# Optimization experiments

Measured on AMD Instinct MI355X. Metric: run time of the kernel, lower is better.

Reference implementation:

```python
import jax, jax.numpy as jnp
import numpy as np

D_MODEL = 2048
NUM_EXPERTS = 64
TOP_K = 2


def setup_inputs() -> dict:
    key = jax.random.key(0)
    k1, k2 = jax.random.split(key)
    x = jax.random.normal(k1, (4, 4096, D_MODEL), dtype=jnp.float32)
    # nn.Linear(d_model, num_experts) weight: [num_experts, d_model]
    W_gate = jax.random.normal(k2, (NUM_EXPERTS, D_MODEL), dtype=jnp.float32) * (1.0 / np.sqrt(D_MODEL))
    return {"x": x, "W_gate": W_gate}


def reference(x, W_gate):
    # logits: [b, s, e]
    logits = jnp.einsum("bsd,ed->bse", x, W_gate)
    probs = jax.nn.softmax(logits, axis=-1)
    expert_weights, expert_indices = jax.lax.top_k(probs, TOP_K)  # [b, s, k]
    expert_weights = expert_weights / jnp.sum(expert_weights, axis=-1, keepdims=True)
    return expert_indices, expert_weights
```

## Files before the change

kernel.cpp:

```cpp
#include <hip/hip_runtime.h>
#include <math.h>

#define NTOK 16384
#define DK   2048
#define NEXP 64

typedef float f32x4 __attribute__((ext_vector_type(4)));
typedef int   i32x4 __attribute__((ext_vector_type(4)));
typedef short s16x8 __attribute__((ext_vector_type(8)));

__device__ __forceinline__ unsigned short f2bf(float f) {
    union { float f; unsigned u; } v; v.f = f;
    unsigned r = (v.u + 0x7FFFu + ((v.u >> 16) & 1u)) >> 16;
    return (unsigned short)r;
}
__device__ __forceinline__ float bf2f(unsigned short h) {
    union { unsigned u; float f; } v; v.u = ((unsigned)h) << 16;
    return v.f;
}

__global__ __launch_bounds__(256) void wsplit_pack(const float* __restrict__ Wg,
                                                   unsigned short* __restrict__ ws) {
    const int t  = blockIdx.x * 256 + threadIdx.x;
    const int e  = t >> 8;
    const int k  = (t & 255) * 8;
    const int w  = k >> 9;
    const int c  = (k >> 5) & 15;
    const int g  = (k >> 3) & 3;
    const int rr = e & 15;
    const int n  = e >> 4;
    const int lane = g * 16 + rr;

    const float* src = Wg + (size_t)e * DK + k;
    unsigned short p0[8], p1[8], p2[8];
    #pragma unroll
    for (int j = 0; j < 8; ++j) {
        const float f = src[j];
        p0[j] = f2bf(f);  const float r1 = f - bf2f(p0[j]);
        p1[j] = f2bf(r1); const float r2 = r1 - bf2f(p1[j]);
        p2[j] = f2bf(r2);
    }
    const size_t base = ((((size_t)w * 16 + c) * 4 + n) * 3) * 512 + (size_t)lane * 8;
    *(s16x8*)(ws + base)        = *(s16x8*)p0;
    *(s16x8*)(ws + base + 512)  = *(s16x8*)p1;
    *(s16x8*)(ws + base + 1024) = *(s16x8*)p2;
}

__device__ __forceinline__ void gload_lds16(const float* src, float* dst) {
    __builtin_amdgcn_global_load_lds(
        (const __attribute__((address_space(1))) void*)src,
        (__attribute__((address_space(3))) void*)dst, 16, 0, 0);
}

__device__ __forceinline__ unsigned cvtpk(float lo, float hi) {
    unsigned r;
    asm("v_cvt_pk_bf16_f32 %0, %1, %2" : "=v"(r) : "v"(lo), "v"(hi));
    return r;
}

#define SPLIT2(F0, F1, O0, O1, O2) { \
    const unsigned q0 = cvtpk((F0), (F1)); \
    const float s0 = (F0) - __builtin_bit_cast(float, q0 << 16); \
    const float s1 = (F1) - __builtin_bit_cast(float, q0 & 0xFFFF0000u); \
    const unsigned q1 = cvtpk(s0, s1); \
    const float t0 = s0 - __builtin_bit_cast(float, q1 << 16); \
    const float t1 = s1 - __builtin_bit_cast(float, q1 & 0xFFFF0000u); \
    O0 = (int)q0; O1 = (int)q1; O2 = (int)cvtpk(t0, t1); }

#define STAGE_X(c, BUF) { \
    _Pragma("unroll") for (int it = 0; it < 4; ++it) \
        gload_lds16(xsrc + (size_t)it * 8 * DK + (size_t)(c) * 32, \
                    &xs[w][BUF][it * 256]); }

#define ISSUE_B(BS, c) { \
    _Pragma("unroll") for (int n = 0; n < 4; ++n) \
        _Pragma("unroll") for (int p = 0; p < 3; ++p) \
            BS[n][p] = *(const i32x4*)(wbase + ((size_t)(c) * 12 + n * 3 + p) * 512); }

#define CONV_LDS(BUF) { \
    _Pragma("unroll") for (int m = 0; m < 2; ++m) { \
        const int row = rr + 16 * m; \
        const int sw  = row & 7; \
        const float4 xa0 = *(const float4*)&xs[w][BUF][row * 32 + (((g * 2 + 0) ^ sw) << 2)]; \
        const float4 xa1 = *(const float4*)&xs[w][BUF][row * 32 + (((g * 2 + 1) ^ sw) << 2)]; \
        SPLIT2(xa0.x, xa0.y, A[m][0].x, A[m][1].x, A[m][2].x); \
        SPLIT2(xa0.z, xa0.w, A[m][0].y, A[m][1].y, A[m][2].y); \
        SPLIT2(xa1.x, xa1.y, A[m][0].z, A[m][1].z, A[m][2].z); \
        SPLIT2(xa1.z, xa1.w, A[m][0].w, A[m][1].w, A[m][2].w); } }

#define MFMA_TERM(pa, pb, BS) { \
    _Pragma("unroll") for (int m = 0; m < 2; ++m) \
        _Pragma("unroll") for (int n = 0; n < 4; ++n) \
            acc[m][n] = __builtin_amdgcn_mfma_f32_16x16x32_bf16( \
                __builtin_bit_cast(s16x8, A[m][pa]), \
                __builtin_bit_cast(s16x8, BS[n][pb]), acc[m][n], 0, 0, 0); }

#define MFMA_ALL(BS) \
    MFMA_TERM(0, 0, BS) MFMA_TERM(0, 1, BS) MFMA_TERM(1, 0, BS) \
    MFMA_TERM(1, 1, BS) MFMA_TERM(0, 2, BS) MFMA_TERM(2, 0, BS)

#define PHASE(BS, c, NCNT, DO_ISSUE) { \
    asm volatile("s_waitcnt vmcnt(" #NCNT ")" ::: "memory"); \
    __builtin_amdgcn_sched_barrier(0); \
    CONV_LDS((c) & 1); \
    MFMA_ALL(BS); \
    if (DO_ISSUE) { STAGE_X((c) + 2, (c) & 1); ISSUE_B(BS, (c) + 2); } \
    __builtin_amdgcn_sched_barrier(0); }

__global__ __launch_bounds__(256, 2) void topk_router_kernel(
    const float* __restrict__ x,
    const unsigned short* __restrict__ ws,
    float* __restrict__ out)
{
    __shared__ float smem[8704];
    float (*xs)[2][1024] = (float (*)[2][1024])smem;
    float (*lg)[32][68]  = (float (*)[32][68])smem;

    const int tid  = threadIdx.x;
    const int w    = tid >> 6;
    const int lane = tid & 63;
    const int rr   = lane & 15;
    const int g    = lane >> 4;
    const int tok0 = blockIdx.x * 32;

    const int lt = lane >> 3;
    const int lq = lane & 7;
    const float* xsrc = x + (size_t)(tok0 + lt) * DK + w * 512 + ((lq ^ lt) * 4);
    const unsigned short* wbase = ws + (size_t)w * 98304 + (size_t)lane * 8;

    f32x4 acc[2][4];
    #pragma unroll
    for (int m = 0; m < 2; ++m)
        #pragma unroll
        for (int n = 0; n < 4; ++n) acc[m][n] = (f32x4){0.f, 0.f, 0.f, 0.f};

    i32x4 B0[4][3], B1[4][3];
    i32x4 A[2][3];

    STAGE_X(0, 0); ISSUE_B(B0, 0);
    STAGE_X(1, 1); ISSUE_B(B1, 1);

    #pragma unroll 1
    for (int c = 0; c < 14; c += 2) {
        PHASE(B0, c,     16, 1);
        PHASE(B1, c + 1, 16, 1);
    }
    PHASE(B0, 14, 16, 0);
    PHASE(B1, 15,  0, 0);

    __syncthreads();
    #pragma unroll
    for (int m = 0; m < 2; ++m)
        #pragma unroll
        for (int n = 0; n < 4; ++n)
            #pragma unroll
            for (int r = 0; r < 4; ++r)
                lg[w][m * 16 + g * 4 + r][n * 16 + rr] = acc[m][n][r];
    __syncthreads();

    #pragma unroll 1
    for (int t = 0; t < 8; ++t) {
        const int tok = w * 8 + t;
        const float v = lg[0][tok][lane] + lg[1][tok][lane]
                      + lg[2][tok][lane] + lg[3][tok][lane];

        float m1 = v; int i1 = lane;
        #pragma unroll
        for (int off = 32; off > 0; off >>= 1) {
            float ov = __shfl_xor(m1, off);
            int   oi = __shfl_xor(i1, off);
            if (ov > m1 || (ov == m1 && oi < i1)) { m1 = ov; i1 = oi; }
        }
        float m2 = (lane == i1) ? -INFINITY : v; int i2 = lane;
        #pragma unroll
        for (int off = 32; off > 0; off >>= 1) {
            float ov = __shfl_xor(m2, off);
            int   oi = __shfl_xor(i2, off);
            if (ov > m2 || (ov == m2 && oi < i2)) { m2 = ov; i2 = oi; }
        }

        if (lane == 0) {
            const int gtok = tok0 + tok;
            const float e  = expf(m2 - m1);
            const float w1 = 1.0f / (1.0f + e);
            const float w2 = e / (1.0f + e);
            out[gtok * 2 + 0] = (float)i1;
            out[gtok * 2 + 1] = (float)i2;
            out[NTOK * 2 + gtok * 2 + 0] = w1;
            out[NTOK * 2 + gtok * 2 + 1] = w2;
        }
    }
}

extern "C" void kernel_launch(void* const* d_in, const int* in_sizes, int n_in,
                              void* d_out, int out_size, void* d_ws, size_t ws_size,
                              hipStream_t stream) {
    const float* x  = (const float*)d_in[0];
    const float* Wg = (const float*)d_in[1];
    float* out = (float*)d_out;
    unsigned short* ws = (unsigned short*)d_ws;
    hipLaunchKernelGGL(wsplit_pack, dim3(64), dim3(256), 0, stream, Wg, ws);
    hipLaunchKernelGGL(topk_router_kernel, dim3(NTOK / 32), dim3(256), 0, stream,
                       x, ws, out);
}
```

Measured before the change: 47.75 us.

## Split K across eight waves per block and load B just-in-time per phase

Doubles the block to 512 threads so eight waves each handle a 256-wide K slice, with eight phases per wave instead of sixteen. The weight layout is flattened so each wave indexes its K rows directly. B fragments now go into a single register buffer loaded at the start of each phase rather than double-buffered two phases ahead, which cuts register pressure to allow more resident waves. The cross-wave reduction grows to eight partials through a padded LDS buffer. The trade-off is that B load latency is no longer hidden by prefetch.

```diff
diff --git a/kernel.cpp b/kernel.cpp
--- a/kernel.cpp
+++ b/kernel.cpp
@@ -24,8 +24,7 @@
     const int t  = blockIdx.x * 256 + threadIdx.x;
     const int e  = t >> 8;
     const int k  = (t & 255) * 8;
-    const int w  = k >> 9;
-    const int c  = (k >> 5) & 15;
+    const int R  = k >> 5;
     const int g  = (k >> 3) & 3;
     const int rr = e & 15;
     const int n  = e >> 4;
@@ -40,7 +39,7 @@
         p1[j] = f2bf(r1); const float r2 = r1 - bf2f(p1[j]);
         p2[j] = f2bf(r2);
     }
-    const size_t base = ((((size_t)w * 16 + c) * 4 + n) * 3) * 512 + (size_t)lane * 8;
+    const size_t base = (((size_t)R * 4 + n) * 3) * 512 + (size_t)lane * 8;
     *(s16x8*)(ws + base)        = *(s16x8*)p0;
     *(s16x8*)(ws + base + 512)  = *(s16x8*)p1;
     *(s16x8*)(ws + base + 1024) = *(s16x8*)p2;
@@ -72,10 +71,10 @@
         gload_lds16(xsrc + (size_t)it * 8 * DK + (size_t)(c) * 32, \
                     &xs[w][BUF][it * 256]); }
 
-#define ISSUE_B(BS, c) { \
+#define ISSUE_B(BS, R) { \
     _Pragma("unroll") for (int n = 0; n < 4; ++n) \
         _Pragma("unroll") for (int p = 0; p < 3; ++p) \
-            BS[n][p] = *(const i32x4*)(wbase + ((size_t)(c) * 12 + n * 3 + p) * 512); }
+            BS[n][p] = *(const i32x4*)(wbase + ((size_t)(R) * 12 + n * 3 + p) * 512); }
 
 #define CONV_LDS(BUF) { \
     _Pragma("unroll") for (int m = 0; m < 2; ++m) { \
@@ -99,22 +98,22 @@
     MFMA_TERM(0, 0, BS) MFMA_TERM(0, 1, BS) MFMA_TERM(1, 0, BS) \
     MFMA_TERM(1, 1, BS) MFMA_TERM(0, 2, BS) MFMA_TERM(2, 0, BS)
 
-#define PHASE(BS, c, NCNT, DO_ISSUE) { \
+#define PHASE(c, NCNT, DO_X) { \
+    ISSUE_B(BS, R0 + (c)); \
     asm volatile("s_waitcnt vmcnt(" #NCNT ")" ::: "memory"); \
     __builtin_amdgcn_sched_barrier(0); \
     CONV_LDS((c) & 1); \
     MFMA_ALL(BS); \
-    if (DO_ISSUE) { STAGE_X((c) + 2, (c) & 1); ISSUE_B(BS, (c) + 2); } \
+    if (DO_X) STAGE_X((c) + 2, (c) & 1); \
     __builtin_amdgcn_sched_barrier(0); }
 
-__global__ __launch_bounds__(256, 2) void topk_router_kernel(
+__global__ __launch_bounds__(512, 4) void topk_router_kernel(
     const float* __restrict__ x,
     const unsigned short* __restrict__ ws,
     float* __restrict__ out)
 {
-    __shared__ float smem[8704];
+    __shared__ float smem[16640];
     float (*xs)[2][1024] = (float (*)[2][1024])smem;
-    float (*lg)[32][68]  = (float (*)[32][68])smem;
 
     const int tid  = threadIdx.x;
     const int w    = tid >> 6;
@@ -122,11 +121,12 @@
     const int rr   = lane & 15;
     const int g    = lane >> 4;
     const int tok0 = blockIdx.x * 32;
+    const int R0   = w * 8;
 
     const int lt = lane >> 3;
     const int lq = lane & 7;
-    const float* xsrc = x + (size_t)(tok0 + lt) * DK + w * 512 + ((lq ^ lt) * 4);
-    const unsigned short* wbase = ws + (size_t)w * 98304 + (size_t)lane * 8;
+    const float* xsrc = x + (size_t)(tok0 + lt) * DK + w * 256 + ((lq ^ lt) * 4);
+    const unsigned short* wbase = ws + (size_t)lane * 8;
 
     f32x4 acc[2][4];
     #pragma unroll
@@ -134,35 +134,41 @@
         #pragma unroll
         for (int n = 0; n < 4; ++n) acc[m][n] = (f32x4){0.f, 0.f, 0.f, 0.f};
 
-    i32x4 B0[4][3], B1[4][3];
+    i32x4 BS[4][3];
     i32x4 A[2][3];
 
-    STAGE_X(0, 0); ISSUE_B(B0, 0);
-    STAGE_X(1, 1); ISSUE_B(B1, 1);
+    STAGE_X(0, 0);
+    STAGE_X(1, 1);
+
+    PHASE(0, 16, 1);
+    PHASE(1, 16, 1);
+    PHASE(2, 16, 1);
+    PHASE(3, 16, 1);
+    PHASE(4, 16, 1);
+    PHASE(5, 16, 1);
+    PHASE(6, 16, 0);
+    PHASE(7, 12, 0);
+
+    __syncthreads();
+    {
+        float* lg = smem;
+        #pragma unroll
+        for (int m = 0; m < 2; ++m)
+            #pragma unroll
+            for (int n = 0; n < 4; ++n)
+                #pragma unroll
+                for (int r = 0; r < 4; ++r)
+                    lg[(w * 32 + m * 16 + g * 4 + r) * 65 + n * 16 + rr]
+                        = acc[m][n][r];
+    }
+    __syncthreads();
 
     #pragma unroll 1
-    for (int c = 0; c < 14; c += 2) {
-        PHASE(B0, c,     16, 1);
-        PHASE(B1, c + 1, 16, 1);
-    }
-    PHASE(B0, 14, 16, 0);
-    PHASE(B1, 15,  0, 0);
-
-    __syncthreads();
-    #pragma unroll
-    for (int m = 0; m < 2; ++m)
-        #pragma unroll
-        for (int n = 0; n < 4; ++n)
-            #pragma unroll
-            for (int r = 0; r < 4; ++r)
-                lg[w][m * 16 + g * 4 + r][n * 16 + rr] = acc[m][n][r];
-    __syncthreads();
-
-    #pragma unroll 1
-    for (int t = 0; t < 8; ++t) {
-        const int tok = w * 8 + t;
-        const float v = lg[0][tok][lane] + lg[1][tok][lane]
-                      + lg[2][tok][lane] + lg[3][tok][lane];
+    for (int t = 0; t < 4; ++t) {
+        const int tok = w * 4 + t;
+        float v = 0.f;
+        #pragma unroll
+        for (int p = 0; p < 8; ++p) v += smem[(p * 32 + tok) * 65 + lane];
 
         float m1 = v; int i1 = lane;
         #pragma unroll
@@ -200,6 +206,6 @@
     float* out = (float*)d_out;
     unsigned short* ws = (unsigned short*)d_ws;
     hipLaunchKernelGGL(wsplit_pack, dim3(64), dim3(256), 0, stream, Wg, ws);
-    hipLaunchKernelGGL(topk_router_kernel, dim3(NTOK / 32), dim3(256), 0, stream,
+    hipLaunchKernelGGL(topk_router_kernel, dim3(NTOK / 32), dim3(512), 0, stream,
                        x, ws, out);
 }
```

Measured after the change: 50.19 us. 1.05x slower.
